# Performance work log

Measured on AMD Instinct MI355X. Metric: run time of the kernel, lower is better.

The kernel has to match this reference:

```python
import jax, jax.numpy as jnp
import numpy as np

B, T, E, H, A, NH = 128, 128, 1024, 1024, 64, 8
SCALE = 1.0 / float(np.sqrt(A))


def setup_inputs() -> dict:
    key = jax.random.key(0)
    ks = jax.random.split(key, 10)
    g = lambda k, shape: jax.random.normal(k, shape, dtype=jnp.float32) * 0.02
    return {
        "encs": jax.random.normal(ks[0], (B, E), dtype=jnp.float32),
        "W_ih": g(ks[1], (3 * H, 2 * E)),
        "W_hh": g(ks[2], (3 * H, H)),
        "b_ih": jnp.zeros((3 * H,), jnp.float32),
        "b_hh": jnp.zeros((3 * H,), jnp.float32),
        "W_mu": g(ks[3], (H, E)),
        "b_mu": jnp.zeros((E,), jnp.float32),
        "W_sig": g(ks[4], (H, E)),
        "b_sig": jnp.zeros((E,), jnp.float32),
        "W_q": g(ks[5], (E, NH * A)),
        "b_q": jnp.zeros((NH * A,), jnp.float32),
        "W_k": g(ks[6], (E, NH * A)),
        "b_k": jnp.zeros((NH * A,), jnp.float32),
        "W_v": g(ks[7], (E, NH * A)),
        "b_v": jnp.zeros((NH * A,), jnp.float32),
        "W_o": g(ks[8], (NH * A, E)),
        "b_o": jnp.zeros((E,), jnp.float32),
    }


def reference(encs, W_ih, W_hh, b_ih, b_hh, W_mu, b_mu, W_sig, b_sig,
              W_q, b_q, W_k, b_k, W_v, b_v, W_o, b_o):
    noise_key = jax.random.key(1234)

    def gru(x, h):  # torch.nn.GRUCell math
        gi = x @ W_ih.T + b_ih
        gh = h @ W_hh.T + b_hh
        ir, iz, inn = jnp.split(gi, 3, axis=-1)
        hr, hz, hn = jnp.split(gh, 3, axis=-1)
        r = jax.nn.sigmoid(ir + hr)
        z = jax.nn.sigmoid(iz + hz)
        n = jnp.tanh(inn + r * hn)
        return (1.0 - z) * n + z * h

    def attn_last(s, i):
        # multi_attn(s,s,s)[:, i]: only row i of softmax is needed (rows independent)
        q = (s[:, :, :] @ W_q + b_q)  # (B,T,NH*A)
        q_i = jax.lax.dynamic_index_in_dim(q, i, axis=1, keepdims=False).reshape(B, NH, A)
        k = (s @ W_k + b_k).reshape(B, T, NH, A)
        v = (s @ W_v + b_v).reshape(B, T, NH, A)
        scores = jnp.einsum("bha,bjha->bhj", q_i, k) * SCALE  # (B,NH,T)
        valid = jnp.arange(T) <= i
        scores = jnp.where(valid[None, None, :], scores, -1e30)
        w = jax.nn.softmax(scores, axis=-1)
        ctx = jnp.einsum("bhj,bjha->bha", w, v).reshape(B, NH * A)
        return ctx @ W_o + b_o  # (B,E)

    def step(carry, i):
        h, mus, sigs, context = carry
        x = jnp.concatenate([encs, context], axis=-1)  # (B,2E)
        h = gru(x, h)
        mu = h @ W_mu + b_mu
        sig = jax.nn.softplus(h @ W_sig + b_sig)
        mus = mus.at[:, i].set(mu)
        sigs = sigs.at[:, i].set(sig)
        eps = jax.random.normal(jax.random.fold_in(noise_key, i), (B, T, E), dtype=jnp.float32)
        valid = (jnp.arange(T) <= i)[None, :, None]
        s = jnp.where(valid, mus + eps * sigs, 0.0)
        context = attn_last(s, i)
        return (h, mus, sigs, context), None

    init = (jnp.zeros((B, H), jnp.float32),
            jnp.zeros((B, T, E), jnp.float32),
            jnp.zeros((B, T, E), jnp.float32),
            jnp.zeros((B, E), jnp.float32))
    (h, mus, sigs, _), _ = jax.lax.scan(step, init, jnp.arange(T))
    # final return is s sampled at step T-1 (all positions valid)
    eps_last = jax.random.normal(jax.random.fold_in(noise_key, T - 1), (B, T, E), dtype=jnp.float32)
    return mus + eps_last * sigs
```

## Files before the change

### kernel.cpp

```cpp
#include <hip/hip_runtime.h>

#define B_   128
#define T_   128
#define E_   1024
#define H_   1024
#define A_   64
#define NH_  8
#define G_   3072
#define QK_  512
#define SCALE_ 0.125f

__device__ __forceinline__ unsigned rotl32(unsigned x, int r) {
  return (x << r) | (x >> (32 - r));
}

__device__ __forceinline__ void tf2x32(unsigned k0, unsigned k1,
                                       unsigned x0, unsigned x1,
                                       unsigned& o0, unsigned& o1) {
  unsigned k2 = k0 ^ k1 ^ 0x1BD11BDAu;
  x0 += k0; x1 += k1;
  x0 += x1; x1 = rotl32(x1, 13); x1 ^= x0;
  x0 += x1; x1 = rotl32(x1, 15); x1 ^= x0;
  x0 += x1; x1 = rotl32(x1, 26); x1 ^= x0;
  x0 += x1; x1 = rotl32(x1,  6); x1 ^= x0;
// ... 129 lines not shown
      WkT[idx] = ld_elem(W_k, (long)e * 512 + qk, isb);
    }
    if (idx < 4096) {
      int j = (int)(idx >> 2), c = (int)(idx & 3);
      float v;
      if (c == 0)      v = bihF[j] + bhhF[j];
      else if (c == 1) v = bihF[1024 + j] + bhhF[1024 + j];
      else if (c == 2) v = bihF[2048 + j];
      else             v = bhhF[2048 + j];
      bias4[idx] = v;
    }
    if (idx < 262144) xh[idx] = 0.f;
    if (idx < 131072) h[idx] = 0.f;
    if (idx < 128) {
      unsigned o0, o1;
      tf2x32(0u, 1234u, 0u, (unsigned)idx, o0, o1);
      skeys[2 * idx] = o0; skeys[2 * idx + 1] = o1;
    }
  } else {
    if (idx < 4194304) {
      int e = (int)(idx & 1023); int col = (int)(idx >> 10);
      int j = col >> 2, c = col & 3;
      float v = 0.f;
      if (c < 3) v = ld_elem(W_ih, (long)(c * 1024 + j) * 2048 + e, isb);
      Wenc4[(long)e * 4096 + col] = v;
    }
  }
}

__global__ __launch_bounds__(256) void consts_kernel(
    const float* __restrict__ bqF, const float* __restrict__ bkF,
    const float* __restrict__ bvF, const float* __restrict__ boF,
    const float* __restrict__ WkT, const float* __restrict__ WoF,
    float* __restrict__ bqk, float* __restrict__ qbc, float* __restrict__ bvo)
{
  int idx = blockIdx.x * 256 + threadIdx.x;
  int hh = idx >> 10, e = idx & 1023;
  float s = 0.f;
  for (int a = 0; a < 64; ++a)
    s += bqF[hh * 64 + a] * WkT[(long)(hh * 64 + a) * 1024 + e];
  bqk[idx] = s;
  if (idx < 1024) {
    float v = boF[idx];
    for (int ha = 0; ha < 512; ++ha) v += bvF[ha] * WoF[(long)ha * 1024 + idx];
    bvo[idx] = v;
  }
  if (idx < 8) {
    float v = 0.f;
    for (int a = 0; a < 64; ++a) v += bqF[idx * 64 + a] * bkF[idx * 64 + a];
    qbc[idx] = v;
  }
}

__global__ __launch_bounds__(256) void mm128(
    const float* __restrict__ A, long lda, long zA, int nsumA, long psA,
    const float* __restrict__ Bm, long ldb, long zB,
    float* __restrict__ C, long ldc, long zC, long pstride,
    int Ktot, int S)
{
  int zz = blockIdx.z;
  int head = zz / S, sp = zz - head * S;
  int Kc = Ktot / S;
  long kb = (long)sp * Kc;
  A += (long)head * zA;
  Bm += (long)head * zB;
  C += (long)head * zC + (long)sp * pstride;
  long m0 = (long)blockIdx.y * 128;
  long n0 = (long)blockIdx.x * 128;
  __shared__ float As[16][132];
  __shared__ float Bs[16][132];
  int tid = threadIdx.x;
  int tx = tid & 15, ty = tid >> 4;
  int am = tid >> 2, ac = tid & 3;
  int bk = tid >> 5, bn = tid & 31;
  float acc[8][8];
  #pragma unroll
  for (int i = 0; i < 8; ++i)
    #pragma unroll
    for (int j = 0; j < 8; ++j) acc[i][j] = 0.f;

  for (int k0 = 0; k0 < Kc; k0 += 16) {
    const float* Ap0 = A + (m0 + am) * lda + kb + k0 + 4 * ac;
    const float* Ap1 = A + (m0 + am + 64) * lda + kb + k0 + 4 * ac;
    float4 a0 = *(const float4*)Ap0;
    float4 a1 = *(const float4*)Ap1;
    for (int s2 = 1; s2 < nsumA; ++s2) {
      float4 t0 = *(const float4*)(Ap0 + (long)s2 * psA);
      float4 t1 = *(const float4*)(Ap1 + (long)s2 * psA);
      a0.x += t0.x; a0.y += t0.y; a0.z += t0.z; a0.w += t0.w;
      a1.x += t1.x; a1.y += t1.y; a1.z += t1.z; a1.w += t1.w;
    }
    float4 b0 = *(const float4*)(Bm + (kb + k0 + bk) * ldb + n0 + 4 * bn);
    float4 b1 = *(const float4*)(Bm + (kb + k0 + bk + 8) * ldb + n0 + 4 * bn);
    __syncthreads();
    As[4 * ac + 0][am] = a0.x; As[4 * ac + 1][am] = a0.y;
    As[4 * ac + 2][am] = a0.z; As[4 * ac + 3][am] = a0.w;
    As[4 * ac + 0][am + 64] = a1.x; As[4 * ac + 1][am + 64] = a1.y;
    As[4 * ac + 2][am + 64] = a1.z; As[4 * ac + 3][am + 64] = a1.w;
    *(float4*)&Bs[bk][4 * bn] = b0;
    *(float4*)&Bs[bk + 8][4 * bn] = b1;
    __syncthreads();
    #pragma unroll
    for (int kk = 0; kk < 16; ++kk) {
      float4 av0 = *(const float4*)&As[kk][ty * 4];
      float4 av1 = *(const float4*)&As[kk][64 + ty * 4];
      float4 bv0 = *(const float4*)&Bs[kk][tx * 4];
      float4 bv1 = *(const float4*)&Bs[kk][64 + tx * 4];
      float amv[8] = {av0.x, av0.y, av0.z, av0.w, av1.x, av1.y, av1.z, av1.w};
      float bnv[8] = {bv0.x, bv0.y, bv0.z, bv0.w, bv1.x, bv1.y, bv1.z, bv1.w};
      #pragma unroll
      for (int i = 0; i < 8; ++i)
        #pragma unroll
        for (int j = 0; j < 8; ++j)
          acc[i][j] = fmaf(amv[i], bnv[j], acc[i][j]);
    }
  }

  #pragma unroll
  for (int i = 0; i < 8; ++i) {
    long r = m0 + (long)(i >> 2) * 64 + ty * 4 + (i & 3);
    float4 v0 = {acc[i][0], acc[i][1], acc[i][2], acc[i][3]};
    float4 v1 = {acc[i][4], acc[i][5], acc[i][6], acc[i][7]};
    *(float4*)(C + r * ldc + n0 + tx * 4) = v0;
    *(float4*)(C + r * ldc + n0 + 64 + tx * 4) = v1;
  }
}

__global__ __launch_bounds__(256) void mm64s(
    const float* __restrict__ A, long lda, long zA,
    const float* __restrict__ Bm, long ldb, long zB,
    float* __restrict__ C, long ldc, long zC, long pstride,
    int Ktot, int S)
{
  int zz = blockIdx.z;
  int head = zz / S, sp = zz - head * S;
  int Kc = Ktot / S;
  long kb = (long)sp * Kc;
  A += (long)head * zA; Bm += (long)head * zB;
  C += (long)head * zC + (long)sp * pstride;
  long n0 = (long)blockIdx.x * 64;
  long m0 = (long)blockIdx.y * 64;
  __shared__ float As[16][68];
  __shared__ float Bs[16][68];
  int tid = threadIdx.x;
  int tx = tid & 15, ty = tid >> 4;
  int ar = tid >> 2, ac = tid & 3;
  int br = tid >> 4, bc = tid & 15;
  float acc[4][4];
  #pragma unroll
  for (int i = 0; i < 4; ++i)
    #pragma unroll
    for (int j = 0; j < 4; ++j) acc[i][j] = 0.f;

  for (int k0 = 0; k0 < Kc; k0 += 16) {
    float4 a4 = *(const float4*)(A + (m0 + ar) * lda + kb + k0 + 4 * ac);
    float4 b4 = *(const float4*)(Bm + (kb + k0 + br) * ldb + n0 + 4 * bc);
    __syncthreads();
    As[4 * ac + 0][ar] = a4.x; As[4 * ac + 1][ar] = a4.y;
    As[4 * ac + 2][ar] = a4.z; As[4 * ac + 3][ar] = a4.w;
    *(float4*)(&Bs[br][4 * bc]) = b4;
    __syncthreads();
    #pragma unroll
    for (int kk = 0; kk < 16; ++kk) {
      float4 av = *(const float4*)(&As[kk][4 * ty]);
      float4 bv = *(const float4*)(&Bs[kk][4 * tx]);
      float amv[4] = {av.x, av.y, av.z, av.w};
      float bnv[4] = {bv.x, bv.y, bv.z, bv.w};
      #pragma unroll
      for (int im = 0; im < 4; ++im)
        #pragma unroll
        for (int jn = 0; jn < 4; ++jn)
          acc[im][jn] = fmaf(amv[im], bnv[jn], acc[im][jn]);
    }
  }
  #pragma unroll
  for (int im = 0; im < 4; ++im) {
    long m = m0 + ty * 4 + im;
    float4 v = {acc[im][0], acc[im][1], acc[im][2], acc[im][3]};
    *(float4*)(C + m * ldc + n0 + tx * 4) = v;
  }
}

__global__ __launch_bounds__(256) void gru_epi(
    const float* __restrict__ gsumP, const float* __restrict__ gie4,
    const float* __restrict__ bias4, float* __restrict__ h,
    float* __restrict__ xh)
{
  int idx = blockIdx.x * 256 + threadIdx.x;
  int b = idx >> 10, j = idx & 1023;
  float4 v = ((const float4*)gie4)[(long)b * 1024 + j];
  float4 bb = ((const float4*)bias4)[j];
  v.x += bb.x; v.y += bb.y; v.z += bb.z; v.w += bb.w;
  #pragma unroll
  for (int s = 0; s < 8; ++s) {
    float4 t = ((const float4*)gsumP)[(long)s * 131072 + (long)b * 1024 + j];
    v.x += t.x; v.y += t.y; v.z += t.z; v.w += t.w;
  }
  float r = sigmoidf_(v.x);
  float z = sigmoidf_(v.y);
  float n = tanhf(v.z + r * v.w);
  float ho = h[idx];
  float hn = (1.0f - z) * n + z * ho;
  h[idx] = hn;
  xh[(long)b * 2048 + 1024 + j] = hn;
}

__global__ __launch_bounds__(256) void musig_epi(
    const float* __restrict__ msP, const float* __restrict__ bmuF,
    const float* __restrict__ bsigF, float* __restrict__ mus,
    float* __restrict__ sigs, int step)
{
  int idx = blockIdx.x * 256 + threadIdx.x;
  int b = idx >> 11, n = idx & 2047;
  float v = 0.f;
  #pragma unroll
  for (int s = 0; s < 8; ++s) v += msP[(long)s * 262144 + idx];
  if (n < 1024) {
    mus[((long)b * T_ + step) * E_ + n] = v + bmuF[n];
  } else {
    float x = v + bsigF[n - 1024];
    sigs[((long)b * T_ + step) * E_ + (n - 1024)] =
        fmaxf(x, 0.0f) + log1pf(expf(-fabsf(x)));
  }
}

__global__ __launch_bounds__(256) void gen_s(
    const float* __restrict__ mus, const float* __restrict__ sigs,
    float* __restrict__ s, const unsigned* __restrict__ skeys, int step)
{
  int t = blockIdx.x;
  int b = blockIdx.y;
  int e = threadIdx.x * 4;
  unsigned sk0 = skeys[2 * step], sk1 = skeys[2 * step + 1];
  unsigned f = (unsigned)(b * (T_ * E_) + t * E_ + e);
  unsigned o0, o1;
  float nv[4];
  tf2x32(sk0, sk1, 0u, f + 0u, o0, o1); nv[0] = bits_to_normal(o0 ^ o1);
  tf2x32(sk0, sk1, 0u, f + 1u, o0, o1); nv[1] = bits_to_normal(o0 ^ o1);
  tf2x32(sk0, sk1, 0u, f + 2u, o0, o1); nv[2] = bits_to_normal(o0 ^ o1);
  tf2x32(sk0, sk1, 0u, f + 3u, o0, o1); nv[3] = bits_to_normal(o0 ^ o1);
  long i4 = (((long)b * T_ + t) * E_ + e) >> 2;
  float4 mu = ((const float4*)mus)[i4];
  float4 sg = ((const float4*)sigs)[i4];
  float4 out;
  out.x = fmaf(nv[0], sg.x, mu.x);
  out.y = fmaf(nv[1], sg.y, mu.y);
  out.z = fmaf(nv[2], sg.z, mu.z);
  out.w = fmaf(nv[3], sg.w, mu.w);
  ((float4*)s)[i4] = out;
}

__global__ __launch_bounds__(256) void t_kernel(
    const float* __restrict__ qP, const float* __restrict__ WkT,
    const float* __restrict__ bkF, const float* __restrict__ bqk,
    const float* __restrict__ qbc, float* __restrict__ tmat,
    float* __restrict__ qb)
{
  int e = blockIdx.x * 256 + threadIdx.x;
  int hh = blockIdx.y;
  int b0 = blockIdx.z * 8;
  __shared__ float q_l[8][64];
  int tid = threadIdx.x;
  for (int idx2 = tid; idx2 < 512; idx2 += 256) {
    int bb = idx2 >> 6, a = idx2 & 63;
    float v = 0.f;
    #pragma unroll
    for (int s = 0; s < 8; ++s)
      v += qP[(long)s * 65536 + (long)(b0 + bb) * 512 + hh * 64 + a];
    q_l[bb][a] = v;
  }
  __syncthreads();
  float acc[8];
  #pragma unroll
  for (int bb = 0; bb < 8; ++bb) acc[bb] = 0.f;
  for (int a = 0; a < 64; ++a) {
    float wv = WkT[(long)(hh * 64 + a) * 1024 + e];
    #pragma unroll
    for (int bb = 0; bb < 8; ++bb) acc[bb] = fmaf(q_l[bb][a], wv, acc[bb]);
  }
  float bq_ = bqk[hh * 1024 + e];
  #pragma unroll
  for (int bb = 0; bb < 8; ++bb)
    tmat[((long)(b0 + bb) * NH_ + hh) * 1024 + e] = acc[bb] + bq_;
  if (blockIdx.x == 0 && tid < 8) {
    int bb = tid;
    float sm = qbc[hh];
    for (int a = 0; a < 64; ++a) sm += q_l[bb][a] * bkF[hh * 64 + a];
    qb[(b0 + bb) * NH_ + hh] = sm;
  }
}

__global__ __launch_bounds__(256) void scores_kernel(
    const float* __restrict__ s, const float* __restrict__ tmat,
    const float* __restrict__ qb, float* __restrict__ scg, int step)
{
  int b = blockIdx.y;
  int jbase = blockIdx.x * 32;
  __shared__ float s_ch[32][132];
  __shared__ float t_ch[8][132];
  int tid = threadIdx.x;
  int hh = tid >> 5, jj = tid & 31;
  int j = jbase + jj;
// ... 30 lines not shown
  if (j <= step)
    scg[((long)b * NH_ + hh) * T_ + j] = (acc + qb[b * NH_ + hh]) * SCALE_;
}

__global__ __launch_bounds__(256) void ctx_kernel(
    const float* __restrict__ s, const float* __restrict__ scg,
    float* __restrict__ ctxE, int step)
{
  int b = blockIdx.y;
  int et = blockIdx.x;
  __shared__ float w_l[NH_][T_];
  __shared__ float s_l[32][68];
  int tid = threadIdx.x;
  {
    int hh = tid >> 5, l = tid & 31;
    const float* sc = scg + ((long)b * NH_ + hh) * T_;
    float m = -3.0e38f;
    for (int j = l; j <= step; j += 32) m = fmaxf(m, sc[j]);
    for (int off = 16; off; off >>= 1) m = fmaxf(m, __shfl_xor(m, off, 32));
    float d = 0.f;
    for (int j = l; j <= step; j += 32) {
      float pe = expf(sc[j] - m);
      w_l[hh][j] = pe;
      d += pe;
    }
    for (int off = 16; off; off >>= 1) d += __shfl_xor(d, off, 32);
    float inv = 1.0f / d;
    for (int j = l; j <= step; j += 32) w_l[hh][j] *= inv;
  }
  int e = tid & 63, hp = tid >> 6;
  float acc0 = 0.f, acc1 = 0.f;
  for (int jc = 0; jc <= step; jc += 32) {
    __syncthreads();
    #pragma unroll
    for (int q = 0; q < 8; ++q) {
      int f = tid + q * 256;
      int jr = f >> 6, ee = f & 63;
      int jg = jc + jr;
      if (jg <= step)
        s_l[jr][ee] = s[((long)b * T_ + jg) * E_ + et * 64 + ee];
    }
    __syncthreads();
    int jmax = min(31, step - jc);
    for (int jr = 0; jr <= jmax; ++jr) {
      float sv = s_l[jr][e];
      acc0 = fmaf(w_l[hp][jc + jr], sv, acc0);
      acc1 = fmaf(w_l[hp + 4][jc + jr], sv, acc1);
    }
  }
  ctxE[((long)b * NH_ + hp) * E_ + et * 64 + e] = acc0;
  ctxE[((long)b * NH_ + hp + 4) * E_ + et * 64 + e] = acc1;
}

__global__ __launch_bounds__(256) void fin_kernel(
    const float* __restrict__ ctxvP, const float* __restrict__ bvo,
    float* __restrict__ xh)
{
  int i4 = blockIdx.x * 256 + threadIdx.x;
  int b = i4 >> 8, e4 = i4 & 255;
  float4 v = ((const float4*)bvo)[e4];
  #pragma unroll
  for (int s = 0; s < 4; ++s) {
    float4 t = ((const float4*)ctxvP)[(long)s * 32768 + (long)b * 256 + e4];
    v.x += t.x; v.y += t.y; v.z += t.z; v.w += t.w;
  }
  ((float4*)xh)[(long)b * 512 + e4] = v;
}

extern "C" void kernel_launch(void* const* d_in, const int* in_sizes, int n_in,
                              void* d_out, int out_size, void* d_ws, size_t ws_size,
                              hipStream_t stream) {
  (void)in_sizes; (void)n_in; (void)out_size; (void)ws_size;
  const void* encs  = d_in[0];
  const void* W_ih  = d_in[1];
  const void* W_hh  = d_in[2];
  const void* b_ih  = d_in[3];
  const void* b_hh  = d_in[4];
  const void* W_mu  = d_in[5];
  const void* b_mu  = d_in[6];
  const void* W_sig = d_in[7];
  const void* b_sig = d_in[8];
  const void* W_q   = d_in[9];
  const void* b_q   = d_in[10];
  const void* W_k   = d_in[11];
  const void* b_k   = d_in[12];
  const void* W_v   = d_in[13];
  const void* b_v   = d_in[14];
  const void* W_o   = d_in[15];
  const void* b_o   = d_in[16];

  float* s = (float*)d_out;
  float* w = (float*)d_ws;

  int*   flag   = (int*)w;
  float* p      = w + 1024;
  float* WbigF  = p;  p += (size_t)2048 * 4096;
  float* WmsF   = p;  p += (size_t)1024 * 2048;
  float* WkTF   = p;  p += (size_t)512 * 1024;
  float* WqF    = p;  p += (size_t)1024 * 512;
  float* WvF    = p;  p += (size_t)1024 * 512;
  float* WoF    = p;  p += (size_t)512 * 1024;
  float* encsF  = p;  p += (size_t)B_ * E_;
  float* bihF   = p;  p += 4096;
  float* bhhF   = p;  p += 4096;
  float* bmuF   = p;  p += 1024;
  float* bsigF  = p;  p += 1024;
  float* bqF    = p;  p += 1024;
  float* bkF    = p;  p += 1024;
  float* bvF    = p;  p += 1024;
  float* boF    = p;  p += 1024;
  float* bias4  = p;  p += 4096;
  float* bqk    = p;  p += 8192;
  float* qbc    = p;  p += 1024;
  float* bvo    = p;  p += 1024;
  unsigned* skeys = (unsigned*)p; p += 1024;
  float* gie4   = p;  p += (size_t)B_ * 4096;
  float* xh     = p;  p += (size_t)B_ * 2048;
  float* hbuf   = p;  p += (size_t)B_ * 1024;
  float* gsumP  = p;  p += (size_t)8 * B_ * 4096;
  float* musigP = p;  p += (size_t)8 * B_ * 2048;
  float* qP     = p;  p += (size_t)8 * B_ * 512;
  float* tmat   = p;  p += (size_t)B_ * NH_ * E_;
  float* qbv    = p;  p += 1024;
  float* scg    = p;  p += (size_t)B_ * NH_ * T_;
  float* ctxE   = p;  p += (size_t)B_ * NH_ * E_;
  float* ctxhP  = p;  p += (size_t)4 * B_ * 512;
  float* ctxvP  = p;  p += (size_t)4 * B_ * 1024;
  float* mus    = p;  p += (size_t)B_ * T_ * E_;
  float* sigs   = p;  p += (size_t)B_ * T_ * E_;
  float* Wenc4  = gsumP;

  sniff_kernel<<<1, 256, 0, stream>>>(encs, flag);
  auto conv = [&](const void* src, float* dst, long n) {
    conv_kernel<<<dim3((unsigned)((n + 255) / 256)), 256, 0, stream>>>(src, dst, n, flag);
  };
  conv(encs,  encsF, (long)B_ * E_);
  conv(b_ih,  bihF,  G_);
  conv(b_hh,  bhhF,  G_);
  conv(b_mu,  bmuF,  1024);
  conv(b_sig, bsigF, 1024);
  conv(b_q,   bqF,   512);
  conv(b_k,   bkF,   512);
  conv(b_v,   bvF,   512);
  conv(b_o,   boF,   1024);
  conv(W_q,   WqF,   (long)1024 * 512);
  conv(W_v,   WvF,   (long)1024 * 512);
  conv(W_o,   WoF,   (long)512 * 1024);

  trans_kernel<<<dim3(16384, 5), 256, 0, stream>>>(
      W_ih, W_hh, W_mu, W_sig, W_k, bihF, bhhF,
      WbigF, WmsF, WkTF, Wenc4, bias4, xh, hbuf, skeys, flag);
  consts_kernel<<<dim3(32), 256, 0, stream>>>(
      bqF, bkF, bvF, boF, WkTF, WoF, bqk, qbc, bvo);
  mm128<<<dim3(32, 1, 1), 256, 0, stream>>>(
      encsF, 1024, 0, 1, 0, Wenc4, 4096, 0, gie4, 4096, 0, 0, 1024, 1);

  for (int i = 0; i < T_; ++i) {
    mm128<<<dim3(32, 1, 8), 256, 0, stream>>>(
        xh, 2048, 0, 1, 0, WbigF, 4096, 0, gsumP, 4096, 0, 524288, 2048, 8);
    gru_epi<<<dim3(512), 256, 0, stream>>>(gsumP, gie4, bias4, hbuf, xh);
    mm128<<<dim3(16, 1, 8), 256, 0, stream>>>(
        hbuf, 1024, 0, 1, 0, WmsF, 2048, 0, musigP, 2048, 0, 262144, 1024, 8);
    musig_epi<<<dim3(1024), 256, 0, stream>>>(musigP, bmuF, bsigF, mus, sigs, i);
    gen_s<<<dim3(i + 1, B_), 256, 0, stream>>>(mus, sigs, s, skeys, i);
    mm128<<<dim3(4, 1, 8), 256, 0, stream>>>(
        s + (long)i * E_, (long)T_ * E_, 0, 1, 0, WqF, 512, 0,
        qP, 512, 0, 65536, 1024, 8);
    t_kernel<<<dim3(4, 8, 16), 256, 0, stream>>>(
        qP, WkTF, bkF, bqk, qbc, tmat, qbv);
    scores_kernel<<<dim3((i + 32) / 32, B_), 256, 0, stream>>>(
        s, tmat, qbv, scg, i);
    ctx_kernel<<<dim3(16, B_), 256, 0, stream>>>(s, scg, ctxE, i);
    mm64s<<<dim3(1, 2, 32), 256, 0, stream>>>(
        ctxE, 8192, 1024, WvF, 512, 64, ctxhP, 512, 64, 65536, 1024, 4);
    mm128<<<dim3(8, 1, 4), 256, 0, stream>>>(
        ctxhP, 512, 0, 4, 65536, WoF, 1024, 0, ctxvP, 1024, 0, 131072, 512, 4);
    fin_kernel<<<dim3(128), 256, 0, stream>>>(ctxvP, bvo, xh);
  }
}
```

Baseline: 27.35 ms.

## Fuse GRU/musig epilogues into following GEMM prologues and overlap noise regeneration

Folds the GRU gate epilogue into the mu/sigma GEMM's A-tile loads, the mu/sigma/softplus/noise sampling into the Q-projection GEMM's A loads, and the split-K reduction plus bias into a single output-projection kernel. The regeneration of earlier s rows is split across extra blocks of the two fused kernels so it runs alongside the GEMMs. This cuts per-step launches from 12 to 8 and avoids the intermediate global round trips. In exchange, the epilogue math is recomputed redundantly across N-tiles, and h is double-buffered to avoid a read/write race.

```diff
diff --git a/kernel.cpp b/kernel.cpp
--- a/kernel.cpp
+++ b/kernel.cpp
@@ -334,73 +334,226 @@
   }
 }
 
-__global__ __launch_bounds__(256) void gru_epi(
+__device__ void gen_rows(int lo, int hi, int lbid, int nb, int step,
+                         const float* __restrict__ mus,
+                         const float* __restrict__ sigs,
+                         float* __restrict__ s,
+                         const unsigned* __restrict__ skeys, int tid) {
+  int nvb = (hi - lo) * 128;
+  if (nvb <= 0) return;
+  unsigned sk0 = skeys[2 * step], sk1 = skeys[2 * step + 1];
+  for (int vb = lbid; vb < nvb; vb += nb) {
+    int t = lo + (vb >> 7);
+    int b = vb & 127;
+    int e = tid * 4;
+    unsigned f = (unsigned)(b * (T_ * E_) + t * E_ + e);
+    unsigned o0, o1;
+    float nv[4];
+    tf2x32(sk0, sk1, 0u, f + 0u, o0, o1); nv[0] = bits_to_normal(o0 ^ o1);
+    tf2x32(sk0, sk1, 0u, f + 1u, o0, o1); nv[1] = bits_to_normal(o0 ^ o1);
+    tf2x32(sk0, sk1, 0u, f + 2u, o0, o1); nv[2] = bits_to_normal(o0 ^ o1);
+    tf2x32(sk0, sk1, 0u, f + 3u, o0, o1); nv[3] = bits_to_normal(o0 ^ o1);
+    long i4 = (((long)b * T_ + t) * E_ + e) >> 2;
+    float4 mu = ((const float4*)mus)[i4];
+    float4 sg = ((const float4*)sigs)[i4];
+    float4 out;
+    out.x = fmaf(nv[0], sg.x, mu.x);
+    out.y = fmaf(nv[1], sg.y, mu.y);
+    out.z = fmaf(nv[2], sg.z, mu.z);
+    out.w = fmaf(nv[3], sg.w, mu.w);
+    ((float4*)s)[i4] = out;
+  }
+}
+
+__device__ __forceinline__ float4 gru4(
     const float* __restrict__ gsumP, const float* __restrict__ gie4,
-    const float* __restrict__ bias4, float* __restrict__ h,
-    float* __restrict__ xh)
-{
-  int idx = blockIdx.x * 256 + threadIdx.x;
-  int b = idx >> 10, j = idx & 1023;
-  float4 v = ((const float4*)gie4)[(long)b * 1024 + j];
-  float4 bb = ((const float4*)bias4)[j];
-  v.x += bb.x; v.y += bb.y; v.z += bb.z; v.w += bb.w;
-  #pragma unroll
-  for (int s = 0; s < 8; ++s) {
-    float4 t = ((const float4*)gsumP)[(long)s * 131072 + (long)b * 1024 + j];
-    v.x += t.x; v.y += t.y; v.z += t.z; v.w += t.w;
-  }
-  float r = sigmoidf_(v.x);
-  float z = sigmoidf_(v.y);
-  float n = tanhf(v.z + r * v.w);
-  float ho = h[idx];
-  float hn = (1.0f - z) * n + z * ho;
-  h[idx] = hn;
-  xh[(long)b * 2048 + 1024 + j] = hn;
-}
-
-__global__ __launch_bounds__(256) void musig_epi(
-    const float* __restrict__ msP, const float* __restrict__ bmuF,
-    const float* __restrict__ bsigF, float* __restrict__ mus,
-    float* __restrict__ sigs, int step)
-{
-  int idx = blockIdx.x * 256 + threadIdx.x;
-  int b = idx >> 11, n = idx & 2047;
-  float v = 0.f;
-  #pragma unroll
-  for (int s = 0; s < 8; ++s) v += msP[(long)s * 262144 + idx];
-  if (n < 1024) {
-    mus[((long)b * T_ + step) * E_ + n] = v + bmuF[n];
-  } else {
-    float x = v + bsigF[n - 1024];
-    sigs[((long)b * T_ + step) * E_ + (n - 1024)] =
-        fmaxf(x, 0.0f) + log1pf(expf(-fabsf(x)));
-  }
-}
-
-__global__ __launch_bounds__(256) void gen_s(
+    const float* __restrict__ bias4, const float* __restrict__ hold,
+    int b, int j0) {
+  float4 ho = *(const float4*)&hold[(long)b * 1024 + j0];
+  float hov[4] = {ho.x, ho.y, ho.z, ho.w};
+  float ov[4];
+  #pragma unroll
+  for (int t = 0; t < 4; ++t) {
+    int j = j0 + t;
+    float4 v = ((const float4*)gie4)[(long)b * 1024 + j];
+    float4 bb = ((const float4*)bias4)[j];
+    v.x += bb.x; v.y += bb.y; v.z += bb.z; v.w += bb.w;
+    #pragma unroll
+    for (int s2 = 0; s2 < 8; ++s2) {
+      float4 tq = ((const float4*)gsumP)[(long)s2 * 131072 + (long)b * 1024 + j];
+      v.x += tq.x; v.y += tq.y; v.z += tq.z; v.w += tq.w;
+    }
+    float r = sigmoidf_(v.x);
+    float z = sigmoidf_(v.y);
+    float n = tanhf(v.z + r * v.w);
+    ov[t] = (1.0f - z) * n + z * hov[t];
+  }
+  float4 out = {ov[0], ov[1], ov[2], ov[3]};
+  return out;
+}
+
+__global__ __launch_bounds__(256) void g2f_kernel(
+    const float* __restrict__ gsumP, const float* __restrict__ gie4,
+    const float* __restrict__ bias4, const float* __restrict__ hold,
+    float* __restrict__ hnew, float* __restrict__ xh,
+    const float* __restrict__ Wms, float* __restrict__ musigP,
     const float* __restrict__ mus, const float* __restrict__ sigs,
     float* __restrict__ s, const unsigned* __restrict__ skeys, int step)
 {
-  int t = blockIdx.x;
-  int b = blockIdx.y;
-  int e = threadIdx.x * 4;
+  int bid = blockIdx.x;
+  int tid = threadIdx.x;
+  if (bid >= 128) {
+    int r1 = (2 * step) / 3;
+    gen_rows(0, r1, bid - 128, 128, step, mus, sigs, s, skeys, tid);
+    return;
+  }
+  int bx = bid & 15, sp = bid >> 4;
+  long kb = (long)sp * 128;
+  long n0 = (long)bx * 128;
+  __shared__ float As[16][132];
+  __shared__ float Bs[16][132];
+  int tx = tid & 15, ty = tid >> 4;
+  int am = tid >> 2, ac = tid & 3;
+  int bk = tid >> 5, bn = tid & 31;
+  float acc[8][8];
+  #pragma unroll
+  for (int i = 0; i < 8; ++i)
+    #pragma unroll
+    for (int j = 0; j < 8; ++j) acc[i][j] = 0.f;
+
+  for (int k0 = 0; k0 < 128; k0 += 16) {
+    int j0 = (int)kb + k0 + 4 * ac;
+    float4 a0 = gru4(gsumP, gie4, bias4, hold, am, j0);
+    float4 a1 = gru4(gsumP, gie4, bias4, hold, am + 64, j0);
+    if (bx == 0) {
+      *(float4*)&hnew[(long)am * 1024 + j0] = a0;
+      *(float4*)&hnew[(long)(am + 64) * 1024 + j0] = a1;
+      *(float4*)&xh[(long)am * 2048 + 1024 + j0] = a0;
+      *(float4*)&xh[(long)(am + 64) * 2048 + 1024 + j0] = a1;
+    }
+    float4 b0 = *(const float4*)(Wms + (kb + k0 + bk) * 2048 + n0 + 4 * bn);
+    float4 b1 = *(const float4*)(Wms + (kb + k0 + bk + 8) * 2048 + n0 + 4 * bn);
+    __syncthreads();
+    As[4 * ac + 0][am] = a0.x; As[4 * ac + 1][am] = a0.y;
+    As[4 * ac + 2][am] = a0.z; As[4 * ac + 3][am] = a0.w;
+    As[4 * ac + 0][am + 64] = a1.x; As[4 * ac + 1][am + 64] = a1.y;
+    As[4 * ac + 2][am + 64] = a1.z; As[4 * ac + 3][am + 64] = a1.w;
+    *(float4*)&Bs[bk][4 * bn] = b0;
+    *(float4*)&Bs[bk + 8][4 * bn] = b1;
+    __syncthreads();
+    #pragma unroll
+    for (int kk = 0; kk < 16; ++kk) {
+      float4 av0 = *(const float4*)&As[kk][ty * 4];
+      float4 av1 = *(const float4*)&As[kk][64 + ty * 4];
+      float4 bv0 = *(const float4*)&Bs[kk][tx * 4];
+      float4 bv1 = *(const float4*)&Bs[kk][64 + tx * 4];
+      float amv[8] = {av0.x, av0.y, av0.z, av0.w, av1.x, av1.y, av1.z, av1.w};
+      float bnv[8] = {bv0.x, bv0.y, bv0.z, bv0.w, bv1.x, bv1.y, bv1.z, bv1.w};
+      #pragma unroll
+      for (int i = 0; i < 8; ++i)
+        #pragma unroll
+        for (int j = 0; j < 8; ++j)
+          acc[i][j] = fmaf(amv[i], bnv[j], acc[i][j]);
+    }
+  }
+
+  float* C = musigP + (long)sp * 262144;
+  #pragma unroll
+  for (int i = 0; i < 8; ++i) {
+    long r = (long)(i >> 2) * 64 + ty * 4 + (i & 3);
+    float4 v0 = {acc[i][0], acc[i][1], acc[i][2], acc[i][3]};
+    float4 v1 = {acc[i][4], acc[i][5], acc[i][6], acc[i][7]};
+    *(float4*)(C + r * 2048 + n0 + tx * 4) = v0;
+    *(float4*)(C + r * 2048 + n0 + 64 + tx * 4) = v1;
+  }
+}
+
+__global__ __launch_bounds__(256) void qf_kernel(
+    const float* __restrict__ musigP, const float* __restrict__ bmuF,
+    const float* __restrict__ bsigF, float* __restrict__ mus,
+    float* __restrict__ sigs, float* __restrict__ s,
+    const float* __restrict__ Wq, float* __restrict__ qP,
+    const unsigned* __restrict__ skeys, int step)
+{
+  int bid = blockIdx.x;
+  int tid = threadIdx.x;
+  if (bid >= 128) {
+    int r1 = (2 * step) / 3;
+    gen_rows(r1, step, bid - 128, 128, step, mus, sigs, s, skeys, tid);
+    return;
+  }
+  int bx = bid & 7, by = (bid >> 3) & 1, sp = bid >> 4;
+  long kb = (long)sp * 128;
+  long n0 = (long)bx * 64;
+  long m0 = (long)by * 64;
+  __shared__ float As[16][68];
+  __shared__ float Bs[16][68];
+  int tx = tid & 15, ty = tid >> 4;
+  int ar = tid >> 2, ac = tid & 3;
+  int br = tid >> 4, bc = tid & 15;
   unsigned sk0 = skeys[2 * step], sk1 = skeys[2 * step + 1];
-  unsigned f = (unsigned)(b * (T_ * E_) + t * E_ + e);
-  unsigned o0, o1;
-  float nv[4];
-  tf2x32(sk0, sk1, 0u, f + 0u, o0, o1); nv[0] = bits_to_normal(o0 ^ o1);
-  tf2x32(sk0, sk1, 0u, f + 1u, o0, o1); nv[1] = bits_to_normal(o0 ^ o1);
-  tf2x32(sk0, sk1, 0u, f + 2u, o0, o1); nv[2] = bits_to_normal(o0 ^ o1);
-  tf2x32(sk0, sk1, 0u, f + 3u, o0, o1); nv[3] = bits_to_normal(o0 ^ o1);
-  long i4 = (((long)b * T_ + t) * E_ + e) >> 2;
-  float4 mu = ((const float4*)mus)[i4];
-  float4 sg = ((const float4*)sigs)[i4];
-  float4 out;
-  out.x = fmaf(nv[0], sg.x, mu.x);
-  out.y = fmaf(nv[1], sg.y, mu.y);
-  out.z = fmaf(nv[2], sg.z, mu.z);
-  out.w = fmaf(nv[3], sg.w, mu.w);
-  ((float4*)s)[i4] = out;
+  float acc[4][4];
+  #pragma unroll
+  for (int i = 0; i < 4; ++i)
+    #pragma unroll
+    for (int j = 0; j < 4; ++j) acc[i][j] = 0.f;
+
+  for (int k0 = 0; k0 < 128; k0 += 16) {
+    int b = (int)m0 + ar;
+    int e0 = (int)kb + k0 + 4 * ac;
+    float4 muq = ((const float4*)bmuF)[e0 >> 2];
+    float4 xgq = ((const float4*)bsigF)[e0 >> 2];
+    #pragma unroll
+    for (int s2 = 0; s2 < 8; ++s2) {
+      float4 tm = ((const float4*)musigP)[((long)s2 * 262144 + (long)b * 2048 + e0) >> 2];
+      float4 tg = ((const float4*)musigP)[((long)s2 * 262144 + (long)b * 2048 + 1024 + e0) >> 2];
+      muq.x += tm.x; muq.y += tm.y; muq.z += tm.z; muq.w += tm.w;
+      xgq.x += tg.x; xgq.y += tg.y; xgq.z += tg.z; xgq.w += tg.w;
+    }
+    float4 sgq;
+    sgq.x = fmaxf(xgq.x, 0.0f) + log1pf(expf(-fabsf(xgq.x)));
+    sgq.y = fmaxf(xgq.y, 0.0f) + log1pf(expf(-fabsf(xgq.y)));
+    sgq.z = fmaxf(xgq.z, 0.0f) + log1pf(expf(-fabsf(xgq.z)));
+    sgq.w = fmaxf(xgq.w, 0.0f) + log1pf(expf(-fabsf(xgq.w)));
+    unsigned f = (unsigned)(b * (T_ * E_) + step * E_ + e0);
+    unsigned o0, o1;
+    float4 a4;
+    tf2x32(sk0, sk1, 0u, f + 0u, o0, o1); a4.x = fmaf(bits_to_normal(o0 ^ o1), sgq.x, muq.x);
+    tf2x32(sk0, sk1, 0u, f + 1u, o0, o1); a4.y = fmaf(bits_to_normal(o0 ^ o1), sgq.y, muq.y);
+    tf2x32(sk0, sk1, 0u, f + 2u, o0, o1); a4.z = fmaf(bits_to_normal(o0 ^ o1), sgq.z, muq.z);
+    tf2x32(sk0, sk1, 0u, f + 3u, o0, o1); a4.w = fmaf(bits_to_normal(o0 ^ o1), sgq.w, muq.w);
+    if (bx == 0) {
+      long o = ((long)b * T_ + step) * E_ + e0;
+      *(float4*)&mus[o] = muq;
+      *(float4*)&sigs[o] = sgq;
+      *(float4*)&s[o] = a4;
+    }
+    float4 b4 = *(const float4*)(Wq + (kb + k0 + br) * 512 + n0 + 4 * bc);
+    __syncthreads();
+    As[4 * ac + 0][ar] = a4.x; As[4 * ac + 1][ar] = a4.y;
+    As[4 * ac + 2][ar] = a4.z; As[4 * ac + 3][ar] = a4.w;
+    *(float4*)(&Bs[br][4 * bc]) = b4;
+    __syncthreads();
+    #pragma unroll
+    for (int kk = 0; kk < 16; ++kk) {
+      float4 av = *(const float4*)(&As[kk][4 * ty]);
+      float4 bv = *(const float4*)(&Bs[kk][4 * tx]);
+      float amv[4] = {av.x, av.y, av.z, av.w};
+      float bnv[4] = {bv.x, bv.y, bv.z, bv.w};
+      #pragma unroll
+      for (int im = 0; im < 4; ++im)
+        #pragma unroll
+        for (int jn = 0; jn < 4; ++jn)
+          acc[im][jn] = fmaf(amv[im], bnv[jn], acc[im][jn]);
+    }
+  }
+  float* C = qP + (long)sp * 65536;
+  #pragma unroll
+  for (int im = 0; im < 4; ++im) {
+    long m = m0 + ty * 4 + im;
+    float4 v = {acc[im][0], acc[im][1], acc[im][2], acc[im][3]};
+    *(float4*)(C + m * 512 + n0 + tx * 4) = v;
+  }
 }
 
 __global__ __launch_bounds__(256) void t_kernel(
@@ -537,19 +690,59 @@
   ctxE[((long)b * NH_ + hp + 4) * E_ + et * 64 + e] = acc1;
 }
 
-__global__ __launch_bounds__(256) void fin_kernel(
-    const float* __restrict__ ctxvP, const float* __restrict__ bvo,
-    float* __restrict__ xh)
-{
-  int i4 = blockIdx.x * 256 + threadIdx.x;
-  int b = i4 >> 8, e4 = i4 & 255;
-  float4 v = ((const float4*)bvo)[e4];
-  #pragma unroll
-  for (int s = 0; s < 4; ++s) {
-    float4 t = ((const float4*)ctxvP)[(long)s * 32768 + (long)b * 256 + e4];
-    v.x += t.x; v.y += t.y; v.z += t.z; v.w += t.w;
-  }
-  ((float4*)xh)[(long)b * 512 + e4] = v;
+__global__ __launch_bounds__(256) void o_kernel(
+    const float* __restrict__ ctxhP, const float* __restrict__ Wo,
+    const float* __restrict__ bvo, float* __restrict__ xh)
+{
+  long n0 = (long)blockIdx.x * 64;
+  long m0 = (long)blockIdx.y * 64;
+  __shared__ float As[16][68];
+  __shared__ float Bs[16][68];
+  int tid = threadIdx.x;
+  int tx = tid & 15, ty = tid >> 4;
+  int ar = tid >> 2, ac = tid & 3;
+  int br = tid >> 4, bc = tid & 15;
+  float acc[4][4];
+  #pragma unroll
+  for (int i = 0; i < 4; ++i)
+    #pragma unroll
+    for (int j = 0; j < 4; ++j) acc[i][j] = 0.f;
+
+  for (int k0 = 0; k0 < 512; k0 += 16) {
+    const float* Ap = ctxhP + (m0 + ar) * 512 + k0 + 4 * ac;
+    float4 a4 = *(const float4*)Ap;
+    #pragma unroll
+    for (int s2 = 1; s2 < 4; ++s2) {
+      float4 t = *(const float4*)(Ap + (long)s2 * 65536);
+      a4.x += t.x; a4.y += t.y; a4.z += t.z; a4.w += t.w;
+    }
+    float4 b4 = *(const float4*)(Wo + (k0 + br) * 1024 + n0 + 4 * bc);
+    __syncthreads();
+    As[4 * ac + 0][ar] = a4.x; As[4 * ac + 1][ar] = a4.y;
+    As[4 * ac + 2][ar] = a4.z; As[4 * ac + 3][ar] = a4.w;
+    *(float4*)(&Bs[br][4 * bc]) = b4;
+    __syncthreads();
+    #pragma unroll
+    for (int kk = 0; kk < 16; ++kk) {
+      float4 av = *(const float4*)(&As[kk][4 * ty]);
+      float4 bv = *(const float4*)(&Bs[kk][4 * tx]);
+      float amv[4] = {av.x, av.y, av.z, av.w};
+      float bnv[4] = {bv.x, bv.y, bv.z, bv.w};
+      #pragma unroll
+      for (int im = 0; im < 4; ++im)
+        #pragma unroll
+        for (int jn = 0; jn < 4; ++jn)
+          acc[im][jn] = fmaf(amv[im], bnv[jn], acc[im][jn]);
+    }
+  }
+  float4 bq = ((const float4*)bvo)[(n0 + tx * 4) >> 2];
+  #pragma unroll
+  for (int im = 0; im < 4; ++im) {
+    long m = m0 + ty * 4 + im;
+    float4 v = {acc[im][0] + bq.x, acc[im][1] + bq.y,
+                acc[im][2] + bq.z, acc[im][3] + bq.w};
+    *(float4*)(xh + m * 2048 + n0 + tx * 4) = v;
+  }
 }
 
 extern "C" void kernel_launch(void* const* d_in, const int* in_sizes, int n_in,
@@ -601,7 +794,8 @@
   unsigned* skeys = (unsigned*)p; p += 1024;
   float* gie4   = p;  p += (size_t)B_ * 4096;
   float* xh     = p;  p += (size_t)B_ * 2048;
-  float* hbuf   = p;  p += (size_t)B_ * 1024;
+  float* hA     = p;  p += (size_t)B_ * 1024;
+  float* hB     = p;  p += (size_t)B_ * 1024;
   float* gsumP  = p;  p += (size_t)8 * B_ * 4096;
   float* musigP = p;  p += (size_t)8 * B_ * 2048;
   float* qP     = p;  p += (size_t)8 * B_ * 512;
@@ -610,7 +804,6 @@
   float* scg    = p;  p += (size_t)B_ * NH_ * T_;
   float* ctxE   = p;  p += (size_t)B_ * NH_ * E_;
   float* ctxhP  = p;  p += (size_t)4 * B_ * 512;
-  float* ctxvP  = p;  p += (size_t)4 * B_ * 1024;
   float* mus    = p;  p += (size_t)B_ * T_ * E_;
   float* sigs   = p;  p += (size_t)B_ * T_ * E_;
   float* Wenc4  = gsumP;
@@ -634,23 +827,21 @@
 
   trans_kernel<<<dim3(16384, 5), 256, 0, stream>>>(
       W_ih, W_hh, W_mu, W_sig, W_k, bihF, bhhF,
-      WbigF, WmsF, WkTF, Wenc4, bias4, xh, hbuf, skeys, flag);
+      WbigF, WmsF, WkTF, Wenc4, bias4, xh, hA, skeys, flag);
   consts_kernel<<<dim3(32), 256, 0, stream>>>(
       bqF, bkF, bvF, boF, WkTF, WoF, bqk, qbc, bvo);
   mm128<<<dim3(32, 1, 1), 256, 0, stream>>>(
       encsF, 1024, 0, 1, 0, Wenc4, 4096, 0, gie4, 4096, 0, 0, 1024, 1);
 
   for (int i = 0; i < T_; ++i) {
+    float* hold = (i & 1) ? hB : hA;
+    float* hnew = (i & 1) ? hA : hB;
     mm128<<<dim3(32, 1, 8), 256, 0, stream>>>(
         xh, 2048, 0, 1, 0, WbigF, 4096, 0, gsumP, 4096, 0, 524288, 2048, 8);
-    gru_epi<<<dim3(512), 256, 0, stream>>>(gsumP, gie4, bias4, hbuf, xh);
-    mm128<<<dim3(16, 1, 8), 256, 0, stream>>>(
-        hbuf, 1024, 0, 1, 0, WmsF, 2048, 0, musigP, 2048, 0, 262144, 1024, 8);
-    musig_epi<<<dim3(1024), 256, 0, stream>>>(musigP, bmuF, bsigF, mus, sigs, i);
-    gen_s<<<dim3(i + 1, B_), 256, 0, stream>>>(mus, sigs, s, skeys, i);
-    mm128<<<dim3(4, 1, 8), 256, 0, stream>>>(
-        s + (long)i * E_, (long)T_ * E_, 0, 1, 0, WqF, 512, 0,
-        qP, 512, 0, 65536, 1024, 8);
+    g2f_kernel<<<dim3(256), 256, 0, stream>>>(
+        gsumP, gie4, bias4, hold, hnew, xh, WmsF, musigP, mus, sigs, s, skeys, i);
+    qf_kernel<<<dim3(256), 256, 0, stream>>>(
+        musigP, bmuF, bsigF, mus, sigs, s, WqF, qP, skeys, i);
     t_kernel<<<dim3(4, 8, 16), 256, 0, stream>>>(
         qP, WkTF, bkF, bqk, qbc, tmat, qbv);
     scores_kernel<<<dim3((i + 32) / 32, B_), 256, 0, stream>>>(
@@ -658,8 +849,6 @@
     ctx_kernel<<<dim3(16, B_), 256, 0, stream>>>(s, scg, ctxE, i);
     mm64s<<<dim3(1, 2, 32), 256, 0, stream>>>(
         ctxE, 8192, 1024, WvF, 512, 64, ctxhP, 512, 64, 65536, 1024, 4);
-    mm128<<<dim3(8, 1, 4), 256, 0, stream>>>(
-        ctxhP, 512, 0, 4, 65536, WoF, 1024, 0, ctxvP, 1024, 0, 131072, 512, 4);
-    fin_kernel<<<dim3(128), 256, 0, stream>>>(ctxvP, bvo, xh);
-  }
-}
+    o_kernel<<<dim3(16, 2), 256, 0, stream>>>(ctxhP, WoF, bvo, xh);
+  }
+}
```

Measured after the change: 38.75 ms. 41.7% more time.

## Overlap noise regeneration with GRU/musig GEMMs and fuse epilogues

Applied to the files above, without the earlier changes.

Regenerates the sampled sequence rows (0..i-1) inside the same launches as the GRU gate GEMM and mu/sigma GEMM, splitting rows two-thirds and one-third between them so the idle CUs do RNG work alongside the GEMM blocks. The new row's noise is produced directly in the mu/sigma epilogue, which removes the separate gen_s launch. The Q projection moves to a smaller-tile GEMM with more blocks, and the output projection plus split-K reduction and bias are fused into one kernel, dropping fin_kernel and the ctxvP buffer. The cost is heterogeneous blocks within each fused kernel and load imbalance when the RNG share is large.

```diff
diff --git a/kernel.cpp b/kernel.cpp
--- a/kernel.cpp
+++ b/kernel.cpp
@@ -205,24 +205,22 @@
   }
 }
 
-__global__ __launch_bounds__(256) void mm128(
-    const float* __restrict__ A, long lda, long zA, int nsumA, long psA,
-    const float* __restrict__ Bm, long ldb, long zB,
-    float* __restrict__ C, long ldc, long zC, long pstride,
-    int Ktot, int S)
-{
-  int zz = blockIdx.z;
+__device__ void mm128_dev(float* smem,
+    const float* A, long lda, long zA, int nsumA, long psA,
+    const float* Bm, long ldb, long zB,
+    float* C, long ldc, long zC, long pstride,
+    int Ktot, int S, int bx, int by, int zz, int tid)
+{
   int head = zz / S, sp = zz - head * S;
   int Kc = Ktot / S;
   long kb = (long)sp * Kc;
   A += (long)head * zA;
   Bm += (long)head * zB;
   C += (long)head * zC + (long)sp * pstride;
-  long m0 = (long)blockIdx.y * 128;
-  long n0 = (long)blockIdx.x * 128;
-  __shared__ float As[16][132];
-  __shared__ float Bs[16][132];
-  int tid = threadIdx.x;
+  long m0 = (long)by * 128;
+  long n0 = (long)bx * 128;
+  float* As = smem;
+  float* Bs = smem + 2112;
   int tx = tid & 15, ty = tid >> 4;
   int am = tid >> 2, ac = tid & 3;
   int bk = tid >> 5, bn = tid & 31;
@@ -246,19 +244,19 @@
     float4 b0 = *(const float4*)(Bm + (kb + k0 + bk) * ldb + n0 + 4 * bn);
     float4 b1 = *(const float4*)(Bm + (kb + k0 + bk + 8) * ldb + n0 + 4 * bn);
     __syncthreads();
-    As[4 * ac + 0][am] = a0.x; As[4 * ac + 1][am] = a0.y;
-    As[4 * ac + 2][am] = a0.z; As[4 * ac + 3][am] = a0.w;
-    As[4 * ac + 0][am + 64] = a1.x; As[4 * ac + 1][am + 64] = a1.y;
-    As[4 * ac + 2][am + 64] = a1.z; As[4 * ac + 3][am + 64] = a1.w;
-    *(float4*)&Bs[bk][4 * bn] = b0;
-    *(float4*)&Bs[bk + 8][4 * bn] = b1;
+    As[(4 * ac + 0) * 132 + am] = a0.x; As[(4 * ac + 1) * 132 + am] = a0.y;
+    As[(4 * ac + 2) * 132 + am] = a0.z; As[(4 * ac + 3) * 132 + am] = a0.w;
+    As[(4 * ac + 0) * 132 + am + 64] = a1.x; As[(4 * ac + 1) * 132 + am + 64] = a1.y;
+    As[(4 * ac + 2) * 132 + am + 64] = a1.z; As[(4 * ac + 3) * 132 + am + 64] = a1.w;
+    *(float4*)&Bs[bk * 132 + 4 * bn] = b0;
+    *(float4*)&Bs[(bk + 8) * 132 + 4 * bn] = b1;
     __syncthreads();
     #pragma unroll
     for (int kk = 0; kk < 16; ++kk) {
-      float4 av0 = *(const float4*)&As[kk][ty * 4];
-      float4 av1 = *(const float4*)&As[kk][64 + ty * 4];
-      float4 bv0 = *(const float4*)&Bs[kk][tx * 4];
-      float4 bv1 = *(const float4*)&Bs[kk][64 + tx * 4];
+      float4 av0 = *(const float4*)&As[kk * 132 + ty * 4];
+      float4 av1 = *(const float4*)&As[kk * 132 + 64 + ty * 4];
+      float4 bv0 = *(const float4*)&Bs[kk * 132 + tx * 4];
+      float4 bv1 = *(const float4*)&Bs[kk * 132 + 64 + tx * 4];
       float amv[8] = {av0.x, av0.y, av0.z, av0.w, av1.x, av1.y, av1.z, av1.w};
       float bnv[8] = {bv0.x, bv0.y, bv0.z, bv0.w, bv1.x, bv1.y, bv1.z, bv1.w};
       #pragma unroll
@@ -277,6 +275,16 @@
     *(float4*)(C + r * ldc + n0 + tx * 4) = v0;
     *(float4*)(C + r * ldc + n0 + 64 + tx * 4) = v1;
   }
+}
+
+__global__ __launch_bounds__(256) void mm128(
+    const float* A, long lda, long zA, int nsumA, long psA,
+    const float* Bm, long ldb, long zB,
+    float* C, long ldc, long zC, long pstride, int Ktot, int S)
+{
+  __shared__ __align__(16) float smem[4224];
+  mm128_dev(smem, A, lda, zA, nsumA, psA, Bm, ldb, zB, C, ldc, zC, pstride,
+            Ktot, S, blockIdx.x, blockIdx.y, blockIdx.z, threadIdx.x);
 }
 
 __global__ __launch_bounds__(256) void mm64s(
@@ -334,6 +342,54 @@
   }
 }
 
+__device__ void gen_rows(int lo, int hi, int lbid, int nb, int step,
+                         const float* __restrict__ mus,
+                         const float* __restrict__ sigs,
+                         float* __restrict__ s,
+                         const unsigned* __restrict__ skeys, int tid) {
+  int nvb = (hi - lo) * 128;
+  if (nvb <= 0) return;
+  unsigned sk0 = skeys[2 * step], sk1 = skeys[2 * step + 1];
+  for (int vb = lbid; vb < nvb; vb += nb) {
+    int t = lo + (vb >> 7);
+    int b = vb & 127;
+    int e = tid * 4;
+    unsigned f = (unsigned)(b * (T_ * E_) + t * E_ + e);
+    unsigned o0, o1;
+    float nv[4];
+    tf2x32(sk0, sk1, 0u, f + 0u, o0, o1); nv[0] = bits_to_normal(o0 ^ o1);
+    tf2x32(sk0, sk1, 0u, f + 1u, o0, o1); nv[1] = bits_to_normal(o0 ^ o1);
+    tf2x32(sk0, sk1, 0u, f + 2u, o0, o1); nv[2] = bits_to_normal(o0 ^ o1);
+    tf2x32(sk0, sk1, 0u, f + 3u, o0, o1); nv[3] = bits_to_normal(o0 ^ o1);
+    long i4 = (((long)b * T_ + t) * E_ + e) >> 2;
+    float4 mu = ((const float4*)mus)[i4];
+    float4 sg = ((const float4*)sigs)[i4];
+    float4 out;
+    out.x = fmaf(nv[0], sg.x, mu.x);
+    out.y = fmaf(nv[1], sg.y, mu.y);
+    out.z = fmaf(nv[2], sg.z, mu.z);
+    out.w = fmaf(nv[3], sg.w, mu.w);
+    ((float4*)s)[i4] = out;
+  }
+}
+
+__global__ __launch_bounds__(256) void g1gen_kernel(
+    const float* __restrict__ xh, const float* __restrict__ Wbig,
+    float* __restrict__ gsumP,
+    const float* __restrict__ mus, const float* __restrict__ sigs,
+    float* __restrict__ s, const unsigned* __restrict__ skeys, int step)
+{
+  __shared__ __align__(16) float smem[4224];
+  int bid = blockIdx.x, tid = threadIdx.x;
+  if (bid < 256) {
+    mm128_dev(smem, xh, 2048, 0, 1, 0, Wbig, 4096, 0,
+              gsumP, 4096, 0, 524288, 2048, 8, bid & 31, 0, bid >> 5, tid);
+  } else {
+    int r1 = (2 * step) / 3;
+    gen_rows(0, r1, bid - 256, 256, step, mus, sigs, s, skeys, tid);
+  }
+}
+
 __global__ __launch_bounds__(256) void gru_epi(
     const float* __restrict__ gsumP, const float* __restrict__ gie4,
     const float* __restrict__ bias4, float* __restrict__ h,
@@ -358,49 +414,46 @@
   xh[(long)b * 2048 + 1024 + j] = hn;
 }
 
-__global__ __launch_bounds__(256) void musig_epi(
-    const float* __restrict__ msP, const float* __restrict__ bmuF,
-    const float* __restrict__ bsigF, float* __restrict__ mus,
-    float* __restrict__ sigs, int step)
-{
-  int idx = blockIdx.x * 256 + threadIdx.x;
-  int b = idx >> 11, n = idx & 2047;
-  float v = 0.f;
-  #pragma unroll
-  for (int s = 0; s < 8; ++s) v += msP[(long)s * 262144 + idx];
-  if (n < 1024) {
-    mus[((long)b * T_ + step) * E_ + n] = v + bmuF[n];
-  } else {
-    float x = v + bsigF[n - 1024];
-    sigs[((long)b * T_ + step) * E_ + (n - 1024)] =
-        fmaxf(x, 0.0f) + log1pf(expf(-fabsf(x)));
-  }
-}
-
-__global__ __launch_bounds__(256) void gen_s(
+__global__ __launch_bounds__(256) void g2gen_kernel(
+    const float* __restrict__ hbuf, const float* __restrict__ Wms,
+    float* __restrict__ musigP,
     const float* __restrict__ mus, const float* __restrict__ sigs,
     float* __restrict__ s, const unsigned* __restrict__ skeys, int step)
 {
-  int t = blockIdx.x;
-  int b = blockIdx.y;
-  int e = threadIdx.x * 4;
+  __shared__ __align__(16) float smem[4224];
+  int bid = blockIdx.x, tid = threadIdx.x;
+  if (bid < 128) {
+    mm128_dev(smem, hbuf, 1024, 0, 1, 0, Wms, 2048, 0,
+              musigP, 2048, 0, 262144, 1024, 8, bid & 15, 0, bid >> 4, tid);
+  } else {
+    int r1 = (2 * step) / 3;
+    gen_rows(r1, step, bid - 128, 128, step, mus, sigs, s, skeys, tid);
+  }
+}
+
+__global__ __launch_bounds__(256) void msgen_kernel(
+    const float* __restrict__ musigP, const float* __restrict__ bmuF,
+    const float* __restrict__ bsigF, float* __restrict__ mus,
+    float* __restrict__ sigs, float* __restrict__ s,
+    const unsigned* __restrict__ skeys, int step)
+{
+  int el = blockIdx.x * 256 + threadIdx.x;
+  int b = el >> 10, e = el & 1023;
+  float mu = bmuF[e], xg = bsigF[e];
+  #pragma unroll
+  for (int s2 = 0; s2 < 8; ++s2) {
+    mu += musigP[(long)s2 * 262144 + (long)b * 2048 + e];
+    xg += musigP[(long)s2 * 262144 + (long)b * 2048 + 1024 + e];
+  }
+  float sig = fmaxf(xg, 0.0f) + log1pf(expf(-fabsf(xg)));
+  long o = ((long)b * T_ + step) * E_ + e;
+  mus[o] = mu;
+  sigs[o] = sig;
   unsigned sk0 = skeys[2 * step], sk1 = skeys[2 * step + 1];
-  unsigned f = (unsigned)(b * (T_ * E_) + t * E_ + e);
+  unsigned f = (unsigned)(b * (T_ * E_) + step * E_ + e);
   unsigned o0, o1;
-  float nv[4];
-  tf2x32(sk0, sk1, 0u, f + 0u, o0, o1); nv[0] = bits_to_normal(o0 ^ o1);
-  tf2x32(sk0, sk1, 0u, f + 1u, o0, o1); nv[1] = bits_to_normal(o0 ^ o1);
-  tf2x32(sk0, sk1, 0u, f + 2u, o0, o1); nv[2] = bits_to_normal(o0 ^ o1);
-  tf2x32(sk0, sk1, 0u, f + 3u, o0, o1); nv[3] = bits_to_normal(o0 ^ o1);
-  long i4 = (((long)b * T_ + t) * E_ + e) >> 2;
-  float4 mu = ((const float4*)mus)[i4];
-  float4 sg = ((const float4*)sigs)[i4];
-  float4 out;
-  out.x = fmaf(nv[0], sg.x, mu.x);
-  out.y = fmaf(nv[1], sg.y, mu.y);
-  out.z = fmaf(nv[2], sg.z, mu.z);
-  out.w = fmaf(nv[3], sg.w, mu.w);
-  ((float4*)s)[i4] = out;
+  tf2x32(sk0, sk1, 0u, f, o0, o1);
+  s[o] = fmaf(bits_to_normal(o0 ^ o1), sig, mu);
 }
 
 __global__ __launch_bounds__(256) void t_kernel(
@@ -537,19 +590,59 @@
   ctxE[((long)b * NH_ + hp + 4) * E_ + et * 64 + e] = acc1;
 }
 
-__global__ __launch_bounds__(256) void fin_kernel(
-    const float* __restrict__ ctxvP, const float* __restrict__ bvo,
-    float* __restrict__ xh)
-{
-  int i4 = blockIdx.x * 256 + threadIdx.x;
-  int b = i4 >> 8, e4 = i4 & 255;
-  float4 v = ((const float4*)bvo)[e4];
-  #pragma unroll
-  for (int s = 0; s < 4; ++s) {
-    float4 t = ((const float4*)ctxvP)[(long)s * 32768 + (long)b * 256 + e4];
-    v.x += t.x; v.y += t.y; v.z += t.z; v.w += t.w;
-  }
-  ((float4*)xh)[(long)b * 512 + e4] = v;
+__global__ __launch_bounds__(256) void o_kernel(
+    const float* __restrict__ ctxhP, const float* __restrict__ Wo,
+    const float* __restrict__ bvo, float* __restrict__ xh)
+{
+  long n0 = (long)blockIdx.x * 64;
+  long m0 = (long)blockIdx.y * 64;
+  __shared__ float As[16][68];
+  __shared__ float Bs[16][68];
+  int tid = threadIdx.x;
+  int tx = tid & 15, ty = tid >> 4;
+  int ar = tid >> 2, ac = tid & 3;
+  int br = tid >> 4, bc = tid & 15;
+  float acc[4][4];
+  #pragma unroll
+  for (int i = 0; i < 4; ++i)
+    #pragma unroll
+    for (int j = 0; j < 4; ++j) acc[i][j] = 0.f;
+
+  for (int k0 = 0; k0 < 512; k0 += 16) {
+    const float* Ap = ctxhP + (m0 + ar) * 512 + k0 + 4 * ac;
+    float4 a4 = *(const float4*)Ap;
+    #pragma unroll
+    for (int s2 = 1; s2 < 4; ++s2) {
+      float4 t = *(const float4*)(Ap + (long)s2 * 65536);
+      a4.x += t.x; a4.y += t.y; a4.z += t.z; a4.w += t.w;
+    }
+    float4 b4 = *(const float4*)(Wo + (k0 + br) * 1024 + n0 + 4 * bc);
+    __syncthreads();
+    As[4 * ac + 0][ar] = a4.x; As[4 * ac + 1][ar] = a4.y;
+    As[4 * ac + 2][ar] = a4.z; As[4 * ac + 3][ar] = a4.w;
+    *(float4*)(&Bs[br][4 * bc]) = b4;
+    __syncthreads();
+    #pragma unroll
+    for (int kk = 0; kk < 16; ++kk) {
+      float4 av = *(const float4*)(&As[kk][4 * ty]);
+      float4 bv = *(const float4*)(&Bs[kk][4 * tx]);
+      float amv[4] = {av.x, av.y, av.z, av.w};
+      float bnv[4] = {bv.x, bv.y, bv.z, bv.w};
+      #pragma unroll
+      for (int im = 0; im < 4; ++im)
+        #pragma unroll
+        for (int jn = 0; jn < 4; ++jn)
+          acc[im][jn] = fmaf(amv[im], bnv[jn], acc[im][jn]);
+    }
+  }
+  float4 bq = ((const float4*)bvo)[(n0 + tx * 4) >> 2];
+  #pragma unroll
+  for (int im = 0; im < 4; ++im) {
+    long m = m0 + ty * 4 + im;
+    float4 v = {acc[im][0] + bq.x, acc[im][1] + bq.y,
+                acc[im][2] + bq.z, acc[im][3] + bq.w};
+    *(float4*)(xh + m * 2048 + n0 + tx * 4) = v;
+  }
 }
 
 extern "C" void kernel_launch(void* const* d_in, const int* in_sizes, int n_in,
@@ -610,7 +703,6 @@
   float* scg    = p;  p += (size_t)B_ * NH_ * T_;
   float* ctxE   = p;  p += (size_t)B_ * NH_ * E_;
   float* ctxhP  = p;  p += (size_t)4 * B_ * 512;
-  float* ctxvP  = p;  p += (size_t)4 * B_ * 1024;
   float* mus    = p;  p += (size_t)B_ * T_ * E_;
   float* sigs   = p;  p += (size_t)B_ * T_ * E_;
   float* Wenc4  = gsumP;
@@ -641,15 +733,15 @@
       encsF, 1024, 0, 1, 0, Wenc4, 4096, 0, gie4, 4096, 0, 0, 1024, 1);
 
   for (int i = 0; i < T_; ++i) {
-    mm128<<<dim3(32, 1, 8), 256, 0, stream>>>(
-        xh, 2048, 0, 1, 0, WbigF, 4096, 0, gsumP, 4096, 0, 524288, 2048, 8);
+    g1gen_kernel<<<dim3(512), 256, 0, stream>>>(
+        xh, WbigF, gsumP, mus, sigs, s, skeys, i);
     gru_epi<<<dim3(512), 256, 0, stream>>>(gsumP, gie4, bias4, hbuf, xh);
-    mm128<<<dim3(16, 1, 8), 256, 0, stream>>>(
-        hbuf, 1024, 0, 1, 0, WmsF, 2048, 0, musigP, 2048, 0, 262144, 1024, 8);
-    musig_epi<<<dim3(1024), 256, 0, stream>>>(musigP, bmuF, bsigF, mus, sigs, i);
-    gen_s<<<dim3(i + 1, B_), 256, 0, stream>>>(mus, sigs, s, skeys, i);
-    mm128<<<dim3(4, 1, 8), 256, 0, stream>>>(
-        s + (long)i * E_, (long)T_ * E_, 0, 1, 0, WqF, 512, 0,
+    g2gen_kernel<<<dim3(256), 256, 0, stream>>>(
+        hbuf, WmsF, musigP, mus, sigs, s, skeys, i);
+    msgen_kernel<<<dim3(512), 256, 0, stream>>>(
+        musigP, bmuF, bsigF, mus, sigs, s, skeys, i);
+    mm64s<<<dim3(8, 2, 8), 256, 0, stream>>>(
+        s + (long)i * E_, (long)T_ * E_, 0, WqF, 512, 0,
         qP, 512, 0, 65536, 1024, 8);
     t_kernel<<<dim3(4, 8, 16), 256, 0, stream>>>(
         qP, WkTF, bkF, bqk, qbc, tmat, qbv);
@@ -658,8 +750,6 @@
     ctx_kernel<<<dim3(16, B_), 256, 0, stream>>>(s, scg, ctxE, i);
     mm64s<<<dim3(1, 2, 32), 256, 0, stream>>>(
         ctxE, 8192, 1024, WvF, 512, 64, ctxhP, 512, 64, 65536, 1024, 4);
-    mm128<<<dim3(8, 1, 4), 256, 0, stream>>>(
-        ctxhP, 512, 0, 4, 65536, WoF, 1024, 0, ctxvP, 1024, 0, 131072, 512, 4);
-    fin_kernel<<<dim3(128), 256, 0, stream>>>(ctxvP, bvo, xh);
-  }
-}
+    o_kernel<<<dim3(16, 2), 256, 0, stream>>>(ctxhP, WoF, bvo, xh);
+  }
+}
```

Measured after the change: 33.83 ms. +23.7%, slower.
